# Performance work log

Hardware: AMD Instinct MI355X
Metric: run time of the kernel (lower is better)

## Reference

```python
import jax, jax.numpy as jnp
import numpy as np

N, E, F, H, C, G = 100000, 800000, 128, 128, 10, 128
EPS = 1e-5


def setup_inputs() -> dict:
    key = jax.random.key(0)
    ks = jax.random.split(key, 8)
    return {
        "x": jax.random.normal(ks[0], (N, F), jnp.float32),
        "edge_index": jax.random.randint(ks[1], (2, E), 0, N),
        "batch": jnp.sort(jax.random.randint(ks[2], (N,), 0, G)),
        "edge_weight": jax.random.uniform(ks[3], (E,), jnp.float32, 0.1, 1.0),
        "bn_feat_w": jnp.ones((F,), jnp.float32),
        "bn_feat_b": jnp.full((F,), 1e-4, jnp.float32),
        "conv_feat_W": jax.random.normal(ks[4], (F, H), jnp.float32) / np.float32(np.sqrt(F)),
        "conv_feat_b": jnp.zeros((H,), jnp.float32),
        "bns_w": jnp.ones((3, H), jnp.float32),
        "bns_b": jnp.full((3, H), 1e-4, jnp.float32),
        "convs_W": jax.random.normal(ks[5], (3, H, H), jnp.float32) / np.float32(np.sqrt(H)),
        "convs_b": jnp.zeros((3, H), jnp.float32),
        "bn_fc_w": jnp.ones((H,), jnp.float32),
        "bn_fc_b": jnp.full((H,), 1e-4, jnp.float32),
        "lin_fc_W": jax.random.normal(ks[6], (H, H), jnp.float32) / np.float32(np.sqrt(H)),
        "lin_fc_b": jnp.zeros((H,), jnp.float32),
        "bn_hidden_w": jnp.ones((H,), jnp.float32),
        "bn_hidden_b": jnp.full((H,), 1e-4, jnp.float32),
        "lin_class_W": jax.random.normal(ks[7], (H, C), jnp.float32) / np.float32(np.sqrt(H)),
        "lin_class_b": jnp.zeros((C,), jnp.float32),
    }


def _bn(h, w, b):
    # training-mode BatchNorm1d: biased batch stats over dim 0
    mu = h.mean(0)
    var = jnp.mean((h - mu) ** 2, 0)
    return (h - mu) * jax.lax.rsqrt(var + EPS) * w + b


def reference(x, edge_index, batch, edge_weight,
              bn_feat_w, bn_feat_b, conv_feat_W, conv_feat_b,
              bns_w, bns_b, convs_W, convs_b,
              bn_fc_w, bn_fc_b, lin_fc_W, lin_fc_b,
              bn_hidden_w, bn_hidden_b, lin_class_W, lin_class_b):
    n = x.shape[0]
    loops = jnp.arange(n)
    # PyG GCNConv: add self-loops (weight 1) + symmetric normalization, shared by all convs
    row = jnp.concatenate([edge_index[0], loops])
    col = jnp.concatenate([edge_index[1], loops])
    ew = jnp.concatenate([edge_weight, jnp.ones((n,), x.dtype)])
    deg = jax.ops.segment_sum(ew, col, num_segments=n)
    dinv = jnp.where(deg > 0, jax.lax.rsqrt(jnp.maximum(deg, EPS)), 0.0)
    norm = (dinv[row] * ew * dinv[col])[:, None]  # [E+N, 1]

    def conv(h, W, b):
        m = (h @ W)[row] * norm                 # gather + scale per edge
        return jax.ops.segment_sum(m, col, num_segments=n) + b

    h = _bn(x, bn_feat_w, bn_feat_b)
    h = jax.nn.relu(conv(h, conv_feat_W, conv_feat_b))
    h_init = h

    x_list = []
    # branch 1: BN -> Conv -> ReLU chain
    h = h_init
    for i in range(3):
        h = jax.nn.relu(conv(_bn(h, bns_w[i], bns_b[i]), convs_W[i], convs_b[i]))
    x_list.append(h)
    # branch 2: double application of the same BN/Conv per step
    h = h_init
    for i in range(3):
        h_ = jax.nn.relu(conv(_bn(h, bns_w[i], bns_b[i]), convs_W[i], convs_b[i]))
        h = jax.nn.relu(conv(_bn(h_, bns_w[i], bns_b[i]), convs_W[i], convs_b[i]))
    x_list.append(h)
    # branch 3: identical to branch 1 when conv_residual=False
    h = h_init
    for i in range(3):
        h = jax.nn.relu(conv(_bn(h, bns_w[i], bns_b[i]), convs_W[i], convs_b[i]))
    x_list.append(h)
    # branch 4: BN -> ReLU only
    h = h_init
    for i in range(3):
        h = jax.nn.relu(_bn(h, bns_w[i], bns_b[i]))
    x_list.append(h)

    def head(hn):
        g = jax.ops.segment_sum(hn, batch, num_segments=G)  # global_add_pool
        g = jax.nn.relu(_bn(g, bn_fc_w, bn_fc_b) @ lin_fc_W + lin_fc_b)
        g = _bn(g, bn_hidden_w, bn_hidden_b)
        return jax.nn.log_softmax(g @ lin_class_W + lin_class_b, axis=-1)

    return tuple(head(hn) for hn in x_list)
```

## Files before the change

### kernel.cpp

```cpp
#include <hip/hip_runtime.h>

#define N_NODES 100000
#define NPAD    100032
#define NBLK    1563
#define NEDGE   800000
#define NGRP    128
#define NSLOT   32
#define EPS     1e-5f

typedef unsigned int   u32;
typedef unsigned short u16;
typedef short bf16x8 __attribute__((ext_vector_type(8)));
typedef float f32x4  __attribute__((ext_vector_type(4)));

__device__ __forceinline__ float bf2f(u32 u){ return __uint_as_float(u << 16); }
__device__ __forceinline__ u16 f2bf(float f){
  u32 x = __float_as_uint(f);
  x += 0x7fffu + ((x >> 16) & 1u);
  return (u16)(x >> 16);
}

__global__ void k_init(float* deg, int* cnt, int* fill, float* gbuf){
  int i = blockIdx.x * 256 + threadIdx.x;
  if (i < NPAD){ deg[i] = 1.0f; cnt[i] = 0; fill[i] = 0; }
  if (i < 4 * NGRP * 128) gbuf[i] = 0.f;
}

__global__ void k_deg(const int* __restrict__ col, const float* __restrict__ ew,
                      float* __restrict__ deg, int* __restrict__ cnt){
  int e = blockIdx.x * 256 + threadIdx.x;
  if (e < NEDGE){
    int c = col[e];
    atomicAdd(&deg[c], ew[e]);
    atomicAdd(&cnt[c], 1);
  }
}

__global__ void k_dinv(const float* __restrict__ deg, float* __restrict__ dinv, float* __restrict__ srow){
  int i = blockIdx.x * 256 + threadIdx.x;
  if (i < N_NODES){
    float d = deg[i];
    float v = d > 0.f ? rsqrtf(fmaxf(d, EPS)) : 0.f;
    dinv[i] = v; srow[i] = v * v;
  }
}

__global__ __launch_bounds__(256) void k_chunksum(const int* __restrict__ cnt, int* __restrict__ csum){
  int b = blockIdx.x, t = threadIdx.x;
  int s = 0;
  for (int i = t; i < 1024; i += 256){ int idx = b * 1024 + i; if (idx < N_NODES) s += cnt[idx]; }
  __shared__ int red[256];
  red[t] = s; __syncthreads();
  for (int o = 128; o > 0; o >>= 1){ if (t < o) red[t] += red[t + o]; __syncthreads(); }
  if (t == 0) csum[b] = red[0];
}

__global__ __launch_bounds__(128) void k_chunkscan(const int* __restrict__ csum, int* __restrict__ coff,
                                                   int* __restrict__ ptrA){
  int t = threadIdx.x;
  __shared__ int s[128];
  int v = (t < 98) ? csum[t] : 0;
  s[t] = v; __syncthreads();
  for (int o = 1; o < 128; o <<= 1){
    int x = (t >= o) ? s[t - o] : 0;
    __syncthreads(); s[t] += x; __syncthreads();
  }
  if (t < 98) coff[t] = s[t] - v;
  if (t == 0) ptrA[N_NODES] = NEDGE;
}

__global__ __launch_bounds__(256) void k_scan2(const int* __restrict__ cnt, const int* __restrict__ coff,
                                               int* __restrict__ ptrA){
  int b = blockIdx.x, t = threadIdx.x;
  int base = b * 1024 + t * 4;
  int v[4], tot = 0;
  #pragma unroll
  for (int k = 0; k < 4; k++){ int idx = base + k; v[k] = (idx < N_NODES) ? cnt[idx] : 0; tot += v[k]; }
  __shared__ int sc[256];
  sc[t] = tot; __syncthreads();
  for (int o = 1; o < 256; o <<= 1){
    int x = (t >= o) ? sc[t - o] : 0;
    __syncthreads(); sc[t] += x; __syncthreads();
  }
  int off = coff[b] + sc[t] - tot;
  #pragma unroll
  for (int k = 0; k < 4; k++){ int idx = base + k; if (idx < N_NODES) ptrA[idx] = off; off += v[k]; }
}

__global__ void k_fill(const int* __restrict__ row, const int* __restrict__ col,
                       const float* __restrict__ ew, const float* __restrict__ dinv,
                       const int* __restrict__ ptrA, int* __restrict__ fill, int2* __restrict__ adj,
                       float* __restrict__ srow){
  int e = blockIdx.x * 256 + threadIdx.x;
  if (e < NEDGE){
    int r = row[e], c = col[e];
    float w = dinv[r] * ew[e] * dinv[c];
    int pos = ptrA[c] + atomicAdd(&fill[c], 1);
    adj[pos] = make_int2(r, __float_as_int(w));
    atomicAdd(&srow[c], w);
  }
}

__global__ __launch_bounds__(256) void k_bhist(const int* __restrict__ batch, int* __restrict__ bpart){
  __shared__ int loc[128];
  int t = threadIdx.x;
  if (t < 128) loc[t] = 0;
  __syncthreads();
  int i = blockIdx.x * 256 + t;
  if (i < N_NODES) atomicAdd(&loc[batch[i]], 1);
  __syncthreads();
  if (t < 128) bpart[blockIdx.x * 128 + t] = loc[t];
}

__global__ __launch_bounds__(128) void k_bscan(const int* __restrict__ bpart, int* __restrict__ gptr){
  int t = threadIdx.x;
  int v = 0;
  for (int p = 0; p < 391; p++) v += bpart[p * 128 + t];
  __shared__ int s[128];
  s[t] = v; __syncthreads();
  for (int o = 1; o < 128; o <<= 1){
    int x = (t >= o) ? s[t - o] : 0;
    __syncthreads(); s[t] += x; __syncthreads();
  }
  gptr[t + 1] = s[t];
  if (t == 0) gptr[0] = 0;
}

__global__ __launch_bounds__(256) void k_cvtstats(const float* __restrict__ x, u32* __restrict__ dst,
                                                  float* __restrict__ sums_out){
  __shared__ float R[1024];
  int t = threadIdx.x;
  float s0 = 0.f, q0 = 0.f, s1 = 0.f, q1 = 0.f;
  size_t base = (size_t)blockIdx.x * 4096 + t;
  #pragma unroll
  for (int it = 0; it < 16; it++){
    size_t idx = base + (size_t)it * 256;
    if (idx < (size_t)N_NODES * 64){
      float2 v = ((const float2*)x)[idx];
      dst[idx] = (u32)f2bf(v.x) | ((u32)f2bf(v.y) << 16);
      s0 += v.x; q0 += v.x * v.x; s1 += v.y; q1 += v.y * v.y;
    }
  }
  R[t] = s0; R[256 + t] = q0; R[512 + t] = s1; R[768 + t] = q1;
  __syncthreads();
  if (t < 64){
    float S0 = 0.f, Q0 = 0.f, S1 = 0.f, Q1 = 0.f;
    #pragma unroll
    for (int g = 0; g < 4; g++){
      S0 += R[g * 64 + t];       Q0 += R[256 + g * 64 + t];
      S1 += R[512 + g * 64 + t]; Q1 += R[768 + g * 64 + t];
    }
    float* so = sums_out + (blockIdx.x & (NSLOT - 1)) * 256;
    atomicAdd(&so[2 * t], S0);
    atomicAdd(&so[2 * t + 1], S1);
    atomicAdd(&so[128 + 2 * t], Q0);
    atomicAdd(&so[128 + 2 * t + 1], Q1);
  }
}

__global__ __launch_bounds__(1024) void k_fold(const float* __restrict__ sums,
    const float* __restrict__ bw, const float* __restrict__ bb,
    const float* __restrict__ W, const float* __restrict__ bias,
    u16* __restrict__ Wh, u16* __restrict__ Wl, float* __restrict__ rb){
  __shared__ float scl[128], shf[128], rbs[128], stot[256];
  int t = threadIdx.x;
  if (t < 256){
    float s = 0.f;
    #pragma unroll 4
    for (int sl = 0; sl < NSLOT; sl++) s += sums[sl * 256 + t];
    stot[t] = s;
  } else if (t < 384) rbs[t - 256] = 0.f;
  __syncthreads();
  if (t < 128){
    float mu  = stot[t] * (1.f / N_NODES);
    float var = stot[128 + t] * (1.f / N_NODES) - mu * mu;
    float sc  = bw[t] * rsqrtf(var + EPS);
    scl[t] = sc; shf[t] = bb[t] - mu * sc;
  }
  __syncthreads();
  #pragma unroll
  for (int r = 0; r < 2; r++){
    int idx = r * 1024 + t;
    int lane_ = idx & 63, sl = idx >> 6;
    int nt_ = sl >> 2, ks_ = sl & 3;
    int n_ = nt_ * 16 + (lane_ & 15);
    int kb = ks_ * 32 + (lane_ >> 4) * 8;
    float rp = 0.f;
    u16 hi8[8], lo8[8];
    #pragma unroll
    for (int j = 0; j < 8; j++){
      float wv = W[(kb + j) * 128 + n_];
      rp += shf[kb + j] * wv;
      float xv = scl[kb + j] * wv;
      u16 hh = f2bf(xv);
      hi8[j] = hh; lo8[j] = f2bf(xv - bf2f(hh));
    }
    uint4 ph, pl;
    ph.x = (u32)hi8[0] | ((u32)hi8[1] << 16); ph.y = (u32)hi8[2] | ((u32)hi8[3] << 16);
    ph.z = (u32)hi8[4] | ((u32)hi8[5] << 16); ph.w = (u32)hi8[6] | ((u32)hi8[7] << 16);
    pl.x = (u32)lo8[0] | ((u32)lo8[1] << 16); pl.y = (u32)lo8[2] | ((u32)lo8[3] << 16);
    pl.z = (u32)lo8[4] | ((u32)lo8[5] << 16); pl.w = (u32)lo8[6] | ((u32)lo8[7] << 16);
    *(uint4*)&Wh[idx * 8] = ph;
    *(uint4*)&Wl[idx * 8] = pl;
    atomicAdd(&rbs[n_], rp);
  }
  __syncthreads();
  if (t < 128){
    rb[t] = rbs[t];
    rb[128 + t] = bias[t];
  }
}

#define CONV_EPILOGUE(RB, HOUT, SOUT)                                          \
  __syncthreads();                                                             \
  sred[t] = 0.f;                                                               \
  __syncthreads();                                                             \
  _Pragma("unroll")                                                            \
  for (int nt = 0; nt < 8; nt++){                                              \
    int colc = nt * 16 + m;                                                    \
    float rv = RB[colc], bv = RB[128 + colc];                                  \
    float s = 0.f, qq = 0.f;                                                   \
    _Pragma("unroll")                                                          \
    for (int r = 0; r < 4; r++){                                               \
      int rown = row0 + q * 4 + r;                                             \
      float v = C[nt][r] + srow[rown] * rv + bv;                               \
      v = fmaxf(v, 0.f);                                                       \
      u16 sv = f2bf(v);                                                        \
      HOUT[(size_t)rown * 128 + colc] = sv;                                    \
      if (rown < N_NODES){ float vv = bf2f(sv); s += vv; qq += vv * vv; }      \
    }                                                                          \
    atomicAdd(&sred[colc], s);                                                 \
    atomicAdd(&sred[128 + colc], qq);                                          \
  }                                                                            \
  __syncthreads();                                                             \
  atomicAdd(&SOUT[(blockIdx.x & (NSLOT - 1)) * 256 + t], sred[t]);

#define GATHER_PHASE()                                                         \
  _Pragma("unroll")                                                            \
  for (int ks = 0; ks < 4; ks++)                                               \
    _Pragma("unroll")                                                          \
    for (int j = 0; j < 8; j++) acc[ks][j] = 0.f;                              \
  if (i < N_NODES){                                                            \
    const u16* hq = h + q * 8;                                                 \
    float di = dinv[i], sw = di * di;                                          \
    _Pragma("unroll")                                                          \
    for (int ks = 0; ks < 4; ks++){                                            \
      uint4 v = *(const uint4*)(hq + (size_t)i * 128 + ks * 32);               \
      acc[ks][0] = sw * __uint_as_float(v.x << 16); acc[ks][1] = sw * __uint_as_float(v.x & 0xffff0000u); \
      acc[ks][2] = sw * __uint_as_float(v.y << 16); acc[ks][3] = sw * __uint_as_float(v.y & 0xffff0000u); \
      acc[ks][4] = sw * __uint_as_float(v.z << 16); acc[ks][5] = sw * __uint_as_float(v.z & 0xffff0000u); \
      acc[ks][6] = sw * __uint_as_float(v.w << 16); acc[ks][7] = sw * __uint_as_float(v.w & 0xffff0000u); \
    }                                                                          \
    int b = ptrA[i], e = ptrA[i + 1];                                          \
    int k = b;                                                                 \
    for (; k + 2 <= e; k += 2){                                                \
      int2 a0 = adj[k], a1 = adj[k + 1];                                       \
      const u16* r0p = hq + (size_t)a0.x * 128;                                \
      const u16* r1p = hq + (size_t)a1.x * 128;                                \
      uint4 u0 = *(const uint4*)(r0p);                                         \
      uint4 u1 = *(const uint4*)(r0p + 32);                                    \
      uint4 u2 = *(const uint4*)(r0p + 64);                                    \
      uint4 u3 = *(const uint4*)(r0p + 96);                                    \
      uint4 w0 = *(const uint4*)(r1p);                                         \
      uint4 w1 = *(const uint4*)(r1p + 32);                                    \
      uint4 w2 = *(const uint4*)(r1p + 64);                                    \
      uint4 w3 = *(const uint4*)(r1p + 96);                                    \
      float f0 = __int_as_float(a0.y), f1 = __int_as_float(a1.y);              \
      FMA_KS(0, u0, f0) FMA_KS(1, u1, f0) FMA_KS(2, u2, f0) FMA_KS(3, u3, f0)  \
      FMA_KS(0, w0, f1) FMA_KS(1, w1, f1) FMA_KS(2, w2, f1) FMA_KS(3, w3, f1)  \
    }                                                                          \
    for (; k < e; k++){                                                        \
      int2 a0 = adj[k];                                                        \
      const u16* r0p = hq + (size_t)a0.x * 128;                                \
      uint4 u0 = *(const uint4*)(r0p);                                         \
      uint4 u1 = *(const uint4*)(r0p + 32);                                    \
      uint4 u2 = *(const uint4*)(r0p + 64);                                    \
      uint4 u3 = *(const uint4*)(r0p + 96);                                    \
      float f0 = __int_as_float(a0.y);                                         \
      FMA_KS(0, u0, f0) FMA_KS(1, u1, f0) FMA_KS(2, u2, f0) FMA_KS(3, u3, f0)  \
    }                                                                          \
  }

#define FMA_KS(KS, V, WT) \
  acc[KS][0] += (WT) * __uint_as_float((V).x << 16); acc[KS][1] += (WT) * __uint_as_float((V).x & 0xffff0000u); \
  acc[KS][2] += (WT) * __uint_as_float((V).y << 16); acc[KS][3] += (WT) * __uint_as_float((V).y & 0xffff0000u); \
  acc[KS][4] += (WT) * __uint_as_float((V).z << 16); acc[KS][5] += (WT) * __uint_as_float((V).z & 0xffff0000u); \
  acc[KS][6] += (WT) * __uint_as_float((V).w << 16); acc[KS][7] += (WT) * __uint_as_float((V).w & 0xffff0000u);

#define MFMA_3PASS(WH, WL_)                                                    \
  _Pragma("unroll")                                                            \
  for (int ks = 0; ks < 4; ks++){                                              \
    _Pragma("unroll")                                                          \
    for (int nt = 0; nt < 8; nt++){                                            \
      bf16x8 bh = ((const bf16x8*)WH)[(nt * 4 + ks) * 64 + lane];              \
      bf16x8 bl = ((const bf16x8*)WL_)[(nt * 4 + ks) * 64 + lane];             \
      C[nt] = __builtin_amdgcn_mfma_f32_16x16x32_bf16(AH[ks], bh, C[nt], 0, 0, 0); \
      C[nt] = __builtin_amdgcn_mfma_f32_16x16x32_bf16(AL[ks], bh, C[nt], 0, 0, 0); \
      C[nt] = __builtin_amdgcn_mfma_f32_16x16x32_bf16(AH[ks], bl, C[nt], 0, 0, 0); \
    }                                                                          \
  }

__global__ __launch_bounds__(256, 4) void k_conv(
    const u16* __restrict__ h, const int* __restrict__ ptrA, const int2* __restrict__ adj,
    const float* __restrict__ dinv, const float* __restrict__ srow,
    const u16* __restrict__ Wh, const u16* __restrict__ Wl, const float* __restrict__ rb,
    u16* __restrict__ hout, float* __restrict__ sums_out){
  __shared__ float sred[256];
  int t = threadIdx.x;
  int wave = t >> 6, lane = t & 63, m = lane & 15, q = lane >> 4;
  int row0 = blockIdx.x * 64 + wave * 16;
  int i = row0 + m;
  float acc[4][8];
  GATHER_PHASE()
  bf16x8 AH[4], AL[4];
  #pragma unroll
  for (int ks = 0; ks < 4; ks++)
    #pragma unroll
    for (int j = 0; j < 8; j++){
      u16 hh = f2bf(acc[ks][j]);
      AH[ks][j] = (short)hh;
      AL[ks][j] = (short)f2bf(acc[ks][j] - bf2f(hh));
    }
  f32x4 C[8];
  #pragma unroll
  for (int nt = 0; nt < 8; nt++) C[nt] = f32x4{0.f, 0.f, 0.f, 0.f};
  MFMA_3PASS(Wh, Wl)
  CONV_EPILOGUE(rb, hout, sums_out)
}

__global__ __launch_bounds__(256, 4) void k_dualconv(
    const u16* __restrict__ h, const int* __restrict__ ptrA, const int2* __restrict__ adj,
    const float* __restrict__ dinv, const float* __restrict__ srow,
    const u16* __restrict__ Wh1, const u16* __restrict__ Wl1, const float* __restrict__ rb1,
    u16* __restrict__ hout1, float* __restrict__ sums1,
    const u16* __restrict__ Wh2, const u16* __restrict__ Wl2, const float* __restrict__ rb2,
    u16* __restrict__ hout2, float* __restrict__ sums2){
  __shared__ float sred[256];
  int t = threadIdx.x;
  int wave = t >> 6, lane = t & 63, m = lane & 15, q = lane >> 4;
  int row0 = blockIdx.x * 64 + wave * 16;
  int i = row0 + m;
  float acc[4][8];
  GATHER_PHASE()
  bf16x8 AH[4], AL[4];
  #pragma unroll
  for (int ks = 0; ks < 4; ks++)
    #pragma unroll
    for (int j = 0; j < 8; j++){
      u16 hh = f2bf(acc[ks][j]);
      AH[ks][j] = (short)hh;
      AL[ks][j] = (short)f2bf(acc[ks][j] - bf2f(hh));
    }
  f32x4 C[8];
  #pragma unroll
  for (int nt = 0; nt < 8; nt++) C[nt] = f32x4{0.f, 0.f, 0.f, 0.f};
  MFMA_3PASS(Wh1, Wl1)
  CONV_EPILOGUE(rb1, hout1, sums1)
  #pragma unroll
  for (int nt = 0; nt < 8; nt++) C[nt] = f32x4{0.f, 0.f, 0.f, 0.f};
  MFMA_3PASS(Wh2, Wl2)
  CONV_EPILOGUE(rb2, hout2, sums2)
}

__global__ __launch_bounds__(256) void k_normrelu(const u16* __restrict__ h, const float* __restrict__ sums,
    const float* __restrict__ bw, const float* __restrict__ bb, u16* __restrict__ o,
    float* __restrict__ sums_out){
  __shared__ float scl[128], shf[128], R[1024], stot[256];
  int t = threadIdx.x;
  {
    float s = 0.f;
    #pragma unroll 4
    for (int sl = 0; sl < NSLOT; sl++) s += sums[sl * 256 + t];
    stot[t] = s;
  }
  __syncthreads();
  if (t < 128){
    float mu  = stot[t] * (1.f / N_NODES);
    float var = stot[128 + t] * (1.f / N_NODES) - mu * mu;
    float sc  = bw[t] * rsqrtf(var + EPS);
    scl[t] = sc; shf[t] = bb[t] - mu * sc;
  }
  __syncthreads();
  int c0 = (t & 63) * 2;
  float sc0 = scl[c0], sh0 = shf[c0], sc1 = scl[c0 + 1], sh1 = shf[c0 + 1];
  float s0 = 0.f, q0 = 0.f, s1 = 0.f, q1 = 0.f;
  size_t base = (size_t)blockIdx.x * 4096 + t;
  #pragma unroll
  for (int it = 0; it < 16; it++){
    size_t idx = base + (size_t)it * 256;
    if (idx < (size_t)N_NODES * 64){
      u32 v = ((const u32*)h)[idx];
      float x0 = fmaxf(bf2f(v & 0xffffu) * sc0 + sh0, 0.f);
      float x1 = fmaxf(bf2f(v >> 16) * sc1 + sh1, 0.f);
      u16 r0 = f2bf(x0), r1 = f2bf(x1);
      ((u32*)o)[idx] = (u32)r0 | ((u32)r1 << 16);
      float y0 = bf2f(r0), y1 = bf2f(r1);
      s0 += y0; q0 += y0 * y0; s1 += y1; q1 += y1 * y1;
    }
  }
  R[t] = s0; R[256 + t] = q0; R[512 + t] = s1; R[768 + t] = q1;
  __syncthreads();
  if (t < 64){
    float S0 = 0.f, Q0 = 0.f, S1 = 0.f, Q1 = 0.f;
    #pragma unroll
    for (int g = 0; g < 4; g++){
      S0 += R[g * 64 + t];       Q0 += R[256 + g * 64 + t];
      S1 += R[512 + g * 64 + t]; Q1 += R[768 + g * 64 + t];
    }
    float* so = sums_out + (blockIdx.x & (NSLOT - 1)) * 256;
    atomicAdd(&so[2 * t], S0);
    atomicAdd(&so[2 * t + 1], S1);
    atomicAdd(&so[128 + 2 * t], Q0);
    atomicAdd(&so[128 + 2 * t + 1], Q1);
  }
}

__global__ __launch_bounds__(128) void k_pool(const u16* __restrict__ h, const int* __restrict__ gptr,
                                              float* __restrict__ gdst){
  int g = blockIdx.x >> 3, s = blockIdx.x & 7, t = threadIdx.x;
  int b = gptr[g], e = gptr[g + 1];
  int len = e - b, per = (len + 7) >> 3;
  int r0 = b + s * per, r1 = min(r0 + per, e);
  float acc = 0.f;
  for (int r = r0; r < r1; r++) acc += bf2f(h[(size_t)r * 128 + t]);
  atomicAdd(&gdst[g * 128 + t], acc);
}

__global__ __launch_bounds__(256) void k_head(const float* __restrict__ gbuf,
    const float* __restrict__ fcw, const float* __restrict__ fcb,
    const float* __restrict__ Wfc, const float* __restrict__ bfc,
    const float* __restrict__ bhw, const float* __restrict__ bhb,
    const float* __restrict__ Wcl, const float* __restrict__ bcl,
    float* __restrict__ out){
  __shared__ float GS[128 * 65];
  __shared__ float ls[256], lq[256];
  __shared__ float scl[128], shf[128], scl2[128], shf2[128];
  __shared__ float sumT[128], sumQ[128];
  __shared__ float WclT[1280], Lrow[1280];
  int t = threadIdx.x, br = blockIdx.x;
  int slot = (br == 1) ? 1 : (br == 3 ? 3 : 0);
  const float* G = gbuf + slot * 16384;
  {
    int col = t & 127, hf2 = t >> 7;
    float s = 0.f, q = 0.f;
    for (int g = hf2 * 64; g < hf2 * 64 + 64; g++){ float v = G[g * 128 + col]; s += v; q += v * v; }
    ls[t] = s; lq[t] = q;
  }
  for (int idx = t; idx < 1280; idx += 256){
    int cc = idx >> 7, c = idx & 127;
    WclT[idx] = Wcl[c * 10 + cc];
  }
  if (t < 128){ sumT[t] = 0.f; sumQ[t] = 0.f; }
  __syncthreads();
  if (t < 128){
    float s = ls[t] + ls[t + 128], q = lq[t] + lq[t + 128];
    float mu = s * (1.f / 128), var = q * (1.f / 128) - mu * mu;
    float sc = fcw[t] * rsqrtf(var + EPS);
    scl[t] = sc; shf[t] = fcb[t] - mu * sc;
  }
  __syncthreads();
  int tr = t >> 4, tc = t & 15, r0 = tr * 8, c0 = tc * 8;
  float acc[8][8];
  #pragma unroll
  for (int a = 0; a < 8; a++)
    #pragma unroll
    for (int b = 0; b < 8; b++) acc[a][b] = 0.f;
  for (int kh = 0; kh < 2; kh++){
    for (int idx = t; idx < 8192; idx += 256){
      int r = idx >> 6, kk = idx & 63, f = kh * 64 + kk;
      GS[r * 65 + kk] = G[r * 128 + f] * scl[f] + shf[f];
    }
    __syncthreads();
    #pragma unroll 2
    for (int k = 0; k < 64; k++){
      float a[8];
      #pragma unroll
      for (int ri = 0; ri < 8; ri++) a[ri] = GS[(r0 + ri) * 65 + k];
      float4 b0 = *(const float4*)&Wfc[(kh * 64 + k) * 128 + c0];
      float4 b1 = *(const float4*)&Wfc[(kh * 64 + k) * 128 + c0 + 4];
      float bb[8] = {b0.x, b0.y, b0.z, b0.w, b1.x, b1.y, b1.z, b1.w};
      #pragma unroll
      for (int ri = 0; ri < 8; ri++)
        #pragma unroll
        for (int ci = 0; ci < 8; ci++) acc[ri][ci] += a[ri] * bb[ci];
    }
    __syncthreads();
  }
  #pragma unroll
  for (int ci = 0; ci < 8; ci++){
    float bb = bfc[c0 + ci];
    float s = 0.f, q = 0.f;
    #pragma unroll
    for (int ri = 0; ri < 8; ri++){
      float v = fmaxf(acc[ri][ci] + bb, 0.f);
      acc[ri][ci] = v; s += v; q += v * v;
    }
    atomicAdd(&sumT[c0 + ci], s);
    atomicAdd(&sumQ[c0 + ci], q);
  }
  __syncthreads();
  if (t < 128){
    float mu = sumT[t] * (1.f / 128), var = sumQ[t] * (1.f / 128) - mu * mu;
    float sc = bhw[t] * rsqrtf(var + EPS);
    scl2[t] = sc; shf2[t] = bhb[t] - mu * sc;
  }
  __syncthreads();
  #pragma unroll
  for (int ci = 0; ci < 8; ci++){
    float sc = scl2[c0 + ci], sh = shf2[c0 + ci];
    #pragma unroll
    for (int ri = 0; ri < 8; ri++) acc[ri][ci] = acc[ri][ci] * sc + sh;
  }
  #pragma unroll
  for (int ri = 0; ri < 8; ri++){
    float pl[10];
    #pragma unroll
    for (int cc = 0; cc < 10; cc++) pl[cc] = 0.f;
    #pragma unroll
    for (int ci = 0; ci < 8; ci++){
      float v = acc[ri][ci];
      #pragma unroll
      for (int cc = 0; cc < 10; cc++) pl[cc] += v * WclT[cc * 128 + c0 + ci];
    }
    #pragma unroll
    for (int msk = 1; msk < 16; msk <<= 1)
      #pragma unroll
      for (int cc = 0; cc < 10; cc++) pl[cc] += __shfl_xor(pl[cc], msk, 64);
    if (tc == 0)
      #pragma unroll
      for (int cc = 0; cc < 10; cc++) Lrow[(r0 + ri) * 10 + cc] = pl[cc];
  }
  __syncthreads();
  if (t < 128){
    float l[10];
    #pragma unroll
    for (int cc = 0; cc < 10; cc++) l[cc] = Lrow[t * 10 + cc] + bcl[cc];
    float m = l[0];
    #pragma unroll
    for (int cc = 1; cc < 10; cc++) m = fmaxf(m, l[cc]);
    float se = 0.f;
    #pragma unroll
    for (int cc = 0; cc < 10; cc++) se += expf(l[cc] - m);
    float lse = m + logf(se);
    #pragma unroll
    for (int cc = 0; cc < 10; cc++) out[br * 1280 + t * 10 + cc] = l[cc] - lse;
  }
}

extern "C" void kernel_launch(void* const* d_in, const int* in_sizes, int n_in,
                              void* d_out, int out_size, void* d_ws, size_t ws_size,
                              hipStream_t stream){
  const float* x    = (const float*)d_in[0];
  const int*  ei    = (const int*)d_in[1];
  const int*  batch = (const int*)d_in[2];
  const float* ew   = (const float*)d_in[3];
  const float* bnfw = (const float*)d_in[4];
  const float* bnfb = (const float*)d_in[5];
  const float* cfW  = (const float*)d_in[6];
  const float* cfb  = (const float*)d_in[7];
  const float* bnsw = (const float*)d_in[8];
  const float* bnsb = (const float*)d_in[9];
  const float* cvW  = (const float*)d_in[10];
  const float* cvb  = (const float*)d_in[11];
  const float* fcw  = (const float*)d_in[12];
  const float* fcb  = (const float*)d_in[13];
  const float* Wfc  = (const float*)d_in[14];
  const float* bfc  = (const float*)d_in[15];
  const float* bhw  = (const float*)d_in[16];
  const float* bhb  = (const float*)d_in[17];
  const float* Wcl  = (const float*)d_in[18];
  const float* bcl  = (const float*)d_in[19];
  float* out = (float*)d_out;

  char* p = (char*)d_ws;
  auto carve = [&](size_t bytes)->void*{ void* r = (void*)p; p += (bytes + 255) & ~(size_t)255; return r; };
  float* deg  = (float*)carve((size_t)NPAD * 4);
  float* dinv = (float*)carve((size_t)NPAD * 4);
  float* srow = (float*)carve((size_t)NPAD * 4);
  int*   cnt  = (int*)carve((size_t)NPAD * 4);
  int*   fill = (int*)carve((size_t)NPAD * 4);
  int*   ptrA = (int*)carve((size_t)(NPAD + 1) * 4);
  int*   bpart= (int*)carve((size_t)391 * 128 * 4);
  int*   csum = (int*)carve(512);
  int*   coff = (int*)carve(512);
  int*   gptr = (int*)carve(1024);
  float* S    = (float*)carve((size_t)13 * NSLOT * 1024);
  float* gbuf = (float*)carve(4 * 128 * 128 * 4);
  u16*   F0h  = (u16*)carve(32768);  u16* F0l = (u16*)carve(32768);  float* F0r = (float*)carve(1024);
  u16*   F1h  = (u16*)carve(32768);  u16* F1l = (u16*)carve(32768);  float* F1r = (float*)carve(1024);
  u16*   F2h  = (u16*)carve(32768);  u16* F2l = (u16*)carve(32768);  float* F2r = (float*)carve(1024);
  u16*   B0   = (u16*)carve((size_t)NPAD * 256);
  u16*   B1   = (u16*)carve((size_t)NPAD * 256);
  u16*   B2   = (u16*)carve((size_t)NPAD * 256);
  u16*   B3   = (u16*)carve((size_t)NPAD * 256);
  int2*  adj  = (int2*)carve((size_t)NEDGE * 8);
  u16*   Xb   = B3;
  auto Sb = [&](int i){ return S + (size_t)i * NSLOT * 256; };

  (void)hipMemsetAsync(S, 0, (size_t)13 * NSLOT * 1024, stream);

  k_init<<<392, 256, 0, stream>>>(deg, cnt, fill, gbuf);
  k_deg<<<3125, 256, 0, stream>>>(ei + NEDGE, ew, deg, cnt);
  k_dinv<<<391, 256, 0, stream>>>(deg, dinv, srow);
  k_chunksum<<<98, 256, 0, stream>>>(cnt, csum);
  k_chunkscan<<<1, 128, 0, stream>>>(csum, coff, ptrA);
  k_scan2<<<98, 256, 0, stream>>>(cnt, coff, ptrA);
  k_fill<<<3125, 256, 0, stream>>>(ei, ei + NEDGE, ew, dinv, ptrA, fill, adj, srow);
  k_bhist<<<391, 256, 0, stream>>>(batch, bpart);
  k_bscan<<<1, 128, 0, stream>>>(bpart, gptr);
  k_cvtstats<<<NBLK, 256, 0, stream>>>(x, (u32*)Xb, Sb(0));

  auto fold = [&](const float* Sin, const float* bw, const float* bb,
                  const float* W, const float* bias, u16* Fh, u16* Fl, float* Fr){
    k_fold<<<1, 1024, 0, stream>>>(Sin, bw, bb, W, bias, Fh, Fl, Fr);
  };
  auto conv = [&](const u16* hin, const u16* Fh, const u16* Fl, const float* Fr,
                  u16* hout, float* Sout){
    k_conv<<<NBLK, 256, 0, stream>>>(hin, ptrA, adj, dinv, srow, Fh, Fl, Fr, hout, Sout);
  };

  fold(Sb(0), bnfw, bnfb, cfW, cfb, F0h, F0l, F0r);
  conv(Xb, F0h, F0l, F0r, B0, Sb(1));
  fold(Sb(1), bnsw, bnsb, cvW, cvb, F1h, F1l, F1r);
  conv(B0, F1h, F1l, F1r, B1, Sb(2));
  k_normrelu<<<NBLK, 256, 0, stream>>>(B0, Sb(1), bnsw,       bnsb,       B2, Sb(3));
  k_normrelu<<<NBLK, 256, 0, stream>>>(B2, Sb(3), bnsw + 128, bnsb + 128, B3, Sb(4));
  k_normrelu<<<NBLK, 256, 0, stream>>>(B3, Sb(4), bnsw + 256, bnsb + 256, B2, Sb(12));
  k_pool<<<1024, 128, 0, stream>>>(B2, gptr, gbuf + 3 * 16384);
  fold(Sb(2), bnsw + 128, bnsb + 128, cvW + 16384, cvb + 128, F0h, F0l, F0r);
  fold(Sb(2), bnsw,       bnsb,       cvW,         cvb,       F1h, F1l, F1r);
  k_dualconv<<<NBLK, 256, 0, stream>>>(B1, ptrA, adj, dinv, srow,
      F0h, F0l, F0r, B3, Sb(5),
      F1h, F1l, F1r, B2, Sb(6));
  fold(Sb(5), bnsw + 256, bnsb + 256, cvW + 32768, cvb + 256, F2h, F2l, F2r);
  conv(B3, F2h, F2l, F2r, B0, Sb(10));
  k_pool<<<1024, 128, 0, stream>>>(B0, gptr, gbuf);
  fold(Sb(6), bnsw + 128, bnsb + 128, cvW + 16384, cvb + 128, F0h, F0l, F0r);
  conv(B2, F0h, F0l, F0r, B1, Sb(7));
  fold(Sb(7), bnsw + 128, bnsb + 128, cvW + 16384, cvb + 128, F1h, F1l, F1r);
  conv(B1, F1h, F1l, F1r, B2, Sb(8));
  fold(Sb(8), bnsw + 256, bnsb + 256, cvW + 32768, cvb + 256, F2h, F2l, F2r);
  conv(B2, F2h, F2l, F2r, B1, Sb(9));
  fold(Sb(9), bnsw + 256, bnsb + 256, cvW + 32768, cvb + 256, F0h, F0l, F0r);
  conv(B1, F0h, F0l, F0r, B3, Sb(11));
  k_pool<<<1024, 128, 0, stream>>>(B3, gptr, gbuf + 16384);

  k_head<<<4, 256, 0, stream>>>(gbuf, fcw, fcb, Wfc, bfc, bhw, bhb, Wcl, bcl, out);
}
```

Baseline: 1.201 ms.

## Gather neighbor rows cooperatively per node and stage aggregates in LDS

Restructures the GCN gather so that each wave processes its 16 rows one node at a time. The 16 column-chunk lanes read contiguous 256-byte neighbor rows, split across 4 edge subsets, with edge indices broadcast by shuffles. Partial sums are reduced with xor-shuffles and written to a padded LDS tile, which is then reread in MFMA fragment layout. The aim is to replace scattered per-lane 64-byte row reads with coalesced row reads and to balance work across lanes. The cost is extra LDS use (about 33KB per block), which may lower occupancy, plus serial per-row loops and shuffle overhead.

```diff
diff --git a/kernel.cpp b/kernel.cpp
--- a/kernel.cpp
+++ b/kernel.cpp
@@ -235,57 +235,81 @@
   __syncthreads();                                                             \
   atomicAdd(&SOUT[(blockIdx.x & (NSLOT - 1)) * 256 + t], sred[t]);
 
-#define GATHER_PHASE()                                                         \
-  _Pragma("unroll")                                                            \
-  for (int ks = 0; ks < 4; ks++)                                               \
-    _Pragma("unroll")                                                          \
-    for (int j = 0; j < 8; j++) acc[ks][j] = 0.f;                              \
-  if (i < N_NODES){                                                            \
-    const u16* hq = h + q * 8;                                                 \
-    float di = dinv[i], sw = di * di;                                          \
+#define FMA8(A, V, W) \
+  A[0] += (W) * __uint_as_float((V).x << 16); A[1] += (W) * __uint_as_float((V).x & 0xffff0000u); \
+  A[2] += (W) * __uint_as_float((V).y << 16); A[3] += (W) * __uint_as_float((V).y & 0xffff0000u); \
+  A[4] += (W) * __uint_as_float((V).z << 16); A[5] += (W) * __uint_as_float((V).z & 0xffff0000u); \
+  A[6] += (W) * __uint_as_float((V).w << 16); A[7] += (W) * __uint_as_float((V).w & 0xffff0000u);
+
+#define HROW_STRIDE 132
+
+__device__ __forceinline__ void gather_lds(const u16* __restrict__ h, const int* __restrict__ ptrA,
+                                           const int2* __restrict__ adj, const float* __restrict__ dinv,
+                                           float* __restrict__ hacc, int row0, int wave, int lane){
+  int s = lane >> 4, c = lane & 15;
+  const u16* hc = h + c * 8;
+  for (int r = 0; r < 16; r++){
+    int i = row0 + r;
+    float a[8] = {0.f, 0.f, 0.f, 0.f, 0.f, 0.f, 0.f, 0.f};
+    if (i < N_NODES){
+      float di = dinv[i], sw = di * di;
+      if (s == 0){
+        uint4 v = *(const uint4*)(hc + (size_t)i * 128);
+        FMA8(a, v, sw)
+      }
+      int b = ptrA[i], e = ptrA[i + 1];
+      for (int kk = b; kk < e; kk += 16){
+        int2 av = make_int2(0, 0);
+        if (kk + c < e) av = adj[kk + c];
+        int jm = min(16, e - kk);
+        int j = s;
+        for (; j + 4 < jm; j += 8){
+          int s0 = __shfl(av.x, j, 64), s1 = __shfl(av.x, j + 4, 64);
+          float w0 = __int_as_float(__shfl(av.y, j, 64));
+          float w1 = __int_as_float(__shfl(av.y, j + 4, 64));
+          uint4 v0 = *(const uint4*)(hc + (size_t)s0 * 128);
+          uint4 v1 = *(const uint4*)(hc + (size_t)s1 * 128);
+          FMA8(a, v0, w0)
+          FMA8(a, v1, w1)
+        }
+        {
+          int s0 = __shfl(av.x, j, 64);
+          float w0 = __int_as_float(__shfl(av.y, j, 64));
+          if (j < jm){
+            uint4 v0 = *(const uint4*)(hc + (size_t)s0 * 128);
+            FMA8(a, v0, w0)
+          }
+        }
+      }
+    }
+    #pragma unroll
+    for (int j = 0; j < 8; j++){
+      a[j] += __shfl_xor(a[j], 16, 64);
+      a[j] += __shfl_xor(a[j], 32, 64);
+    }
+    int rowb = (wave * 16 + r) * HROW_STRIDE + c * 8;
+    if (s == 0) *(float4*)&hacc[rowb]     = make_float4(a[0], a[1], a[2], a[3]);
+    if (s == 1) *(float4*)&hacc[rowb + 4] = make_float4(a[4], a[5], a[6], a[7]);
+  }
+}
+
+#define BUILD_AFRAG()                                                          \
+  bf16x8 AH[4], AL[4];                                                         \
+  {                                                                            \
+    const float* sp = &hacc[(wave * 16 + m) * HROW_STRIDE + q * 8];            \
     _Pragma("unroll")                                                          \
     for (int ks = 0; ks < 4; ks++){                                            \
-      uint4 v = *(const uint4*)(hq + (size_t)i * 128 + ks * 32);               \
-      acc[ks][0] = sw * __uint_as_float(v.x << 16); acc[ks][1] = sw * __uint_as_float(v.x & 0xffff0000u); \
-      acc[ks][2] = sw * __uint_as_float(v.y << 16); acc[ks][3] = sw * __uint_as_float(v.y & 0xffff0000u); \
-      acc[ks][4] = sw * __uint_as_float(v.z << 16); acc[ks][5] = sw * __uint_as_float(v.z & 0xffff0000u); \
-      acc[ks][6] = sw * __uint_as_float(v.w << 16); acc[ks][7] = sw * __uint_as_float(v.w & 0xffff0000u); \
+      float4 x0 = *(const float4*)(sp + ks * 32);                              \
+      float4 x1 = *(const float4*)(sp + ks * 32 + 4);                          \
+      float av8[8] = {x0.x, x0.y, x0.z, x0.w, x1.x, x1.y, x1.z, x1.w};         \
+      _Pragma("unroll")                                                        \
+      for (int j = 0; j < 8; j++){                                             \
+        u16 hh = f2bf(av8[j]);                                                 \
+        AH[ks][j] = (short)hh;                                                 \
+        AL[ks][j] = (short)f2bf(av8[j] - bf2f(hh));                            \
+      }                                                                        \
     }                                                                          \
-    int b = ptrA[i], e = ptrA[i + 1];                                          \
-    int k = b;                                                                 \
-    for (; k + 2 <= e; k += 2){                                                \
-      int2 a0 = adj[k], a1 = adj[k + 1];                                       \
-      const u16* r0p = hq + (size_t)a0.x * 128;                                \
-      const u16* r1p = hq + (size_t)a1.x * 128;                                \
-      uint4 u0 = *(const uint4*)(r0p);                                         \
-      uint4 u1 = *(const uint4*)(r0p + 32);                                    \
-      uint4 u2 = *(const uint4*)(r0p + 64);                                    \
-      uint4 u3 = *(const uint4*)(r0p + 96);                                    \
-      uint4 w0 = *(const uint4*)(r1p);                                         \
-      uint4 w1 = *(const uint4*)(r1p + 32);                                    \
-      uint4 w2 = *(const uint4*)(r1p + 64);                                    \
-      uint4 w3 = *(const uint4*)(r1p + 96);                                    \
-      float f0 = __int_as_float(a0.y), f1 = __int_as_float(a1.y);              \
-      FMA_KS(0, u0, f0) FMA_KS(1, u1, f0) FMA_KS(2, u2, f0) FMA_KS(3, u3, f0)  \
-      FMA_KS(0, w0, f1) FMA_KS(1, w1, f1) FMA_KS(2, w2, f1) FMA_KS(3, w3, f1)  \
-    }                                                                          \
-    for (; k < e; k++){                                                        \
-      int2 a0 = adj[k];                                                        \
-      const u16* r0p = hq + (size_t)a0.x * 128;                                \
-      uint4 u0 = *(const uint4*)(r0p);                                         \
-      uint4 u1 = *(const uint4*)(r0p + 32);                                    \
-      uint4 u2 = *(const uint4*)(r0p + 64);                                    \
-      uint4 u3 = *(const uint4*)(r0p + 96);                                    \
-      float f0 = __int_as_float(a0.y);                                         \
-      FMA_KS(0, u0, f0) FMA_KS(1, u1, f0) FMA_KS(2, u2, f0) FMA_KS(3, u3, f0)  \
-    }                                                                          \
-  }
-
-#define FMA_KS(KS, V, WT) \
-  acc[KS][0] += (WT) * __uint_as_float((V).x << 16); acc[KS][1] += (WT) * __uint_as_float((V).x & 0xffff0000u); \
-  acc[KS][2] += (WT) * __uint_as_float((V).y << 16); acc[KS][3] += (WT) * __uint_as_float((V).y & 0xffff0000u); \
-  acc[KS][4] += (WT) * __uint_as_float((V).z << 16); acc[KS][5] += (WT) * __uint_as_float((V).z & 0xffff0000u); \
-  acc[KS][6] += (WT) * __uint_as_float((V).w << 16); acc[KS][7] += (WT) * __uint_as_float((V).w & 0xffff0000u);
+  }
 
 #define MFMA_3PASS(WH, WL_)                                                    \
   _Pragma("unroll")                                                            \
@@ -305,22 +329,14 @@
     const float* __restrict__ dinv, const float* __restrict__ srow,
     const u16* __restrict__ Wh, const u16* __restrict__ Wl, const float* __restrict__ rb,
     u16* __restrict__ hout, float* __restrict__ sums_out){
+  __shared__ float hacc[64 * HROW_STRIDE];
   __shared__ float sred[256];
   int t = threadIdx.x;
   int wave = t >> 6, lane = t & 63, m = lane & 15, q = lane >> 4;
   int row0 = blockIdx.x * 64 + wave * 16;
-  int i = row0 + m;
-  float acc[4][8];
-  GATHER_PHASE()
-  bf16x8 AH[4], AL[4];
-  #pragma unroll
-  for (int ks = 0; ks < 4; ks++)
-    #pragma unroll
-    for (int j = 0; j < 8; j++){
-      u16 hh = f2bf(acc[ks][j]);
-      AH[ks][j] = (short)hh;
-      AL[ks][j] = (short)f2bf(acc[ks][j] - bf2f(hh));
-    }
+  gather_lds(h, ptrA, adj, dinv, hacc, row0, wave, lane);
+  __syncthreads();
+  BUILD_AFRAG()
   f32x4 C[8];
   #pragma unroll
   for (int nt = 0; nt < 8; nt++) C[nt] = f32x4{0.f, 0.f, 0.f, 0.f};
@@ -335,22 +351,14 @@
     u16* __restrict__ hout1, float* __restrict__ sums1,
     const u16* __restrict__ Wh2, const u16* __restrict__ Wl2, const float* __restrict__ rb2,
     u16* __restrict__ hout2, float* __restrict__ sums2){
+  __shared__ float hacc[64 * HROW_STRIDE];
   __shared__ float sred[256];
   int t = threadIdx.x;
   int wave = t >> 6, lane = t & 63, m = lane & 15, q = lane >> 4;
   int row0 = blockIdx.x * 64 + wave * 16;
-  int i = row0 + m;
-  float acc[4][8];
-  GATHER_PHASE()
-  bf16x8 AH[4], AL[4];
-  #pragma unroll
-  for (int ks = 0; ks < 4; ks++)
-    #pragma unroll
-    for (int j = 0; j < 8; j++){
-      u16 hh = f2bf(acc[ks][j]);
-      AH[ks][j] = (short)hh;
-      AL[ks][j] = (short)f2bf(acc[ks][j] - bf2f(hh));
-    }
+  gather_lds(h, ptrA, adj, dinv, hacc, row0, wave, lane);
+  __syncthreads();
+  BUILD_AFRAG()
   f32x4 C[8];
   #pragma unroll
   for (int nt = 0; nt < 8; nt++) C[nt] = f32x4{0.f, 0.f, 0.f, 0.f};
```

Result: slower. 1.540 ms (+28.2%).
